# Optimization experiments

Measured on AMD Instinct MI355X. Metric: run time of the kernel, lower is better.

## Reference

```python
import jax, jax.numpy as jnp
import numpy as np

ANCHORS = [[(116, 90), (156, 198), (373, 326)],
           [(30, 61), (62, 45), (59, 119)],
           [(10, 13), (16, 30), (33, 23)]]
STRIDES = [32, 16, 8]
NC = 80            # num_classes
SCORE_THRESH = 0.01
NMS_THRESH = 0.45
TOPK = 200
PRE_NMS = 400


def _decode_level(feat, anchors, stride):
    # feat: [B, A*(NC+5), H, W]
    bs, C, H, W = feat.shape
    A = len(anchors)
    p = feat.reshape(bs, A, NC + 5, H, W).transpose(0, 1, 3, 4, 2)  # b a h w c
    gx = jnp.arange(W, dtype=feat.dtype)
    gy = jnp.arange(H, dtype=feat.dtype)
    aw = jnp.asarray([a[0] for a in anchors], feat.dtype)  # anchor w in pixels
    ah = jnp.asarray([a[1] for a in anchors], feat.dtype)
    # (sigmoid(x)+grid)*stride ; exp(w)*(anchor/stride)*stride = exp(w)*anchor
    bx = (jax.nn.sigmoid(p[..., 0]) + gx[None, None, None, :]) * stride
    by = (jax.nn.sigmoid(p[..., 1]) + gy[None, None, :, None]) * stride
    bw = jnp.exp(p[..., 2]) * aw[None, :, None, None]
    bh = jnp.exp(p[..., 3]) * ah[None, :, None, None]
    conf = jax.nn.sigmoid(p[..., 4])
    cls = jax.nn.sigmoid(p[..., 5:])
    out = jnp.concatenate([jnp.stack([bx, by, bw, bh, conf], -1), cls], -1)
    return out.reshape(bs, A * H * W, NC + 5)


def _iou_matrix(boxes):
    # boxes: [K,4] xyxy -> [K,K] IoU
    x1, y1, x2, y2 = boxes[:, 0], boxes[:, 1], boxes[:, 2], boxes[:, 3]
    area = jnp.maximum(x2 - x1, 0.0) * jnp.maximum(y2 - y1, 0.0)
    ix1 = jnp.maximum(x1[:, None], x1[None, :])
    iy1 = jnp.maximum(y1[:, None], y1[None, :])
    ix2 = jnp.minimum(x2[:, None], x2[None, :])
    iy2 = jnp.minimum(y2[:, None], y2[None, :])
    inter = jnp.maximum(ix2 - ix1, 0.0) * jnp.maximum(iy2 - iy1, 0.0)
    union = area[:, None] + area[None, :] - inter
    return inter / jnp.maximum(union, 1e-9)


def _nms_single(pred):
    # pred: [N, 5+NC] with xyxy boxes in cols 0:4, obj conf col 4, class probs 5:
    N = pred.shape[0]
    scores = pred[:, 4:5] * pred[:, 5:]                 # [N, NC]
    flat = scores.reshape(-1)                            # [N*NC]
    flat = jnp.where(flat >= SCORE_THRESH, flat, -1.0)   # low scores sink to bottom
    vals, idx = jax.lax.top_k(flat, PRE_NMS)             # [PRE_NMS]
    box_idx = idx // NC
    cls_idx = idx % NC
    boxes = pred[box_idx, :4]                            # [PRE_NMS, 4]
    valid = vals >= SCORE_THRESH

    iou = _iou_matrix(boxes)
    same_cls = cls_idx[:, None] == cls_idx[None, :]
    later = jnp.arange(PRE_NMS)[None, :] > jnp.arange(PRE_NMS)[:, None]
    sup_mat = (iou > NMS_THRESH) & same_cls & later      # [K,K] i suppresses j

    def body(i, keep):
        sup = sup_mat[i] & keep[i] & valid[i]
        return keep & (~sup)

    keep = jax.lax.fori_loop(0, PRE_NMS, body, jnp.ones(PRE_NMS, bool))
    keep = keep & valid

    final = jnp.where(keep, vals, -1.0)
    sel_scores, sel = jax.lax.top_k(final, TOPK)         # kept boxes, score-sorted
    pad = sel_scores < 0.0
    out_boxes = jnp.where(pad[:, None], 0.0, boxes[sel])
    out_scores = jnp.where(pad, 0.0, sel_scores)
    out_labels = jnp.where(pad, -1.0, cls_idx[sel].astype(pred.dtype))
    return jnp.concatenate([out_boxes, out_scores[:, None], out_labels[:, None]], -1)


def _forward(feat0, feat1, feat2):
    preds = [_decode_level(f, a, s) for f, a, s in
             zip((feat0, feat1, feat2), ANCHORS, STRIDES)]
    pred = jnp.concatenate(preds, axis=1)                # [B, Ntot, 5+NC]
    cx, cy, w, h = pred[..., 0], pred[..., 1], pred[..., 2], pred[..., 3]
    corners = jnp.stack([cx - w / 2, cy - h / 2, cx + w / 2, cy + h / 2], -1)
    pred = jnp.concatenate([corners, pred[..., 4:]], -1)
    return jax.vmap(_nms_single)(pred)                   # [B, TOPK, 6]


def setup_inputs() -> dict:
    key = jax.random.key(0)
    k0, k1, k2 = jax.random.split(key, 3)
    return {
        "feat0": jax.random.normal(k0, (8, 255, 19, 19), jnp.float32),
        "feat1": jax.random.normal(k1, (8, 255, 38, 38), jnp.float32),
        "feat2": jax.random.normal(k2, (8, 255, 76, 76), jnp.float32),
    }


def reference(feat0, feat1, feat2):
    return _forward(feat0, feat1, feat2)
```

## Files before the change

kernel.cpp:

```cpp
#include <hip/hip_runtime.h>
#include <stdint.h>

#define NB      22743
#define L0N     1083
#define L1N     5415
#define PRE     400
#define TOPK_N  200
#define CAP     2048
#define NBATCH  8
#define NBINS1  2048
#define NBINS2  4096
#define MIN_VALID_P9 (0xBC23D70Au >> 9)

typedef unsigned long long u64;
typedef unsigned int u32;

__device__ __forceinline__ float sigf(float x) { return 1.0f / (1.0f + expf(-x)); }

__device__ __forceinline__ u32 mono32(float f) {
    u32 u = __float_as_uint(f);
    return (u & 0x80000000u) ? ~u : (u | 0x80000000u);
}
__device__ __forceinline__ float unmono(u32 m) {
    u32 u = (m & 0x80000000u) ? (m & 0x7FFFFFFFu) : ~m;
    return __uint_as_float(u);
}

__device__ __forceinline__ const float* box_base(
    const float* f0, const float* f1, const float* f2,
    int b, int g, int* HW, int* cw, int* ch, float* stride, float* aw, float* ah)
{
    const float* f; int W, off, li;
    if (g < L0N)      { f = f0; W = 19; off = 0;   li = 0; *stride = 32.f; }
    else if (g < L1N) { f = f1; W = 38; off = L0N; li = 1; *stride = 16.f; }
    else              { f = f2; W = 76; off = L1N; li = 2; *stride = 8.f;  }
    const float AWt[3][3] = {{116.f,156.f,373.f},{30.f,62.f,59.f},{10.f,16.f,33.f}};
    const float AHt[3][3] = {{90.f,198.f,326.f},{61.f,45.f,119.f},{13.f,30.f,23.f}};
    int hw = W * W;
    int local = g - off;
    int a = local / hw; int r = local - a * hw;
    int h = r / W; int w = r - h * W;
    *HW = hw; *cw = w; *ch = h;
    *aw = AWt[li][a]; *ah = AHt[li][a];
    return f + (size_t)((b * 255 + a * 85) * hw + h * W + w);
}

template<int MODE>
__global__ void score_pass(const float* __restrict__ f0, const float* __restrict__ f1,
                           const float* __restrict__ f2,
                           u32* __restrict__ ghist, const int2* __restrict__ sel1,
                           const u32* __restrict__ t23, u32* __restrict__ cnt,
                           u64* __restrict__ cand)
{
    __shared__ u32 h[(MODE == 0) ? NBINS1 * 4 : ((MODE == 1) ? NBINS2 : 1)];
    const int b = blockIdx.y;
    const int tid = threadIdx.x;
    if (MODE == 0) { for (int i = tid; i < NBINS1 * 4; i += 256) h[i] = 0; __syncthreads(); }
    if (MODE == 1) { for (int i = tid; i < NBINS2; i += 256) h[i] = 0; __syncthreads(); }

    const int g = blockIdx.x * blockDim.x + tid;
    if (g < NB) {
        int HW, cw, ch; float stride, aw, ah;
        const float* p = box_base(f0, f1, f2, b, g, &HW, &cw, &ch, &stride, &aw, &ah);
        float conf = sigf(p[4 * HW]);
        u32 b1 = 0, T = 0;
        if (MODE == 1) b1 = (u32)sel1[b].x;
        if (MODE == 2) T = t23[b];
        bool do_box;
        if (MODE == 0)      do_box = (conf >= 0.01f);
        else if (MODE == 1) do_box = ((mono32(conf) >> 21) >= b1);
        else                do_box = ((mono32(conf) >> 9)  >= T);
        if (do_box) {
            for (int c = 0; c < 80; ++c) {
                float s = conf * sigf(p[(5 + c) * HW]);
                if (s < 0.01f) continue;
                u32 m = mono32(s);
                if (MODE == 0) {
                    atomicAdd(&h[(m >> 21) * 4 + (tid & 3)], 1u);
                } else if (MODE == 1) {
                    if ((m >> 21) == b1) atomicAdd(&h[(m >> 9) & 0xFFFu], 1u);
                } else {
                    if ((m >> 9) >= T) {
                        u32 pos = atomicAdd(&cnt[b], 1u);
                        if (pos < CAP) {
                            u32 e = (u32)(g * 80 + c);
                            cand[b * CAP + pos] = ((u64)m << 32) | (u64)(0xFFFFFFFFu - e);
                        }
                    }
                }
            }
        }
    }
    if (MODE == 0) {
        __syncthreads();
        u32* gh = ghist + b * NBINS1;
        for (int i = tid; i < NBINS1; i += 256) {
            u32 s = h[i*4] + h[i*4+1] + h[i*4+2] + h[i*4+3];
            if (s) atomicAdd(&gh[i], s);
        }
    }
    if (MODE == 1) {
        __syncthreads();
        u32* gh = ghist + b * NBINS2;
        for (int i = tid; i < NBINS2; i += 256)
            if (h[i]) atomicAdd(&gh[i], h[i]);
    }
}

template<int LEVEL>
__global__ __launch_bounds__(256) void scan_k(const u32* __restrict__ ghist,
                                              int2* __restrict__ sel1,
                                              u32* __restrict__ t23)
{
    constexpr int NB_ = (LEVEL == 1) ? NBINS1 : NBINS2;
    constexpr int CH  = NB_ / 256;
    const int b = blockIdx.x;
    const int tid = threadIdx.x;
    const u32* h = ghist + b * NB_;
    __shared__ u32 lh[NB_];
    __shared__ u32 part[256];
    __shared__ u32 suf[256];

    const u32 need = (LEVEL == 1) ? (u32)PRE : (u32)(PRE - sel1[b].y);

    for (int i = tid; i < NB_; i += 256) lh[i] = h[i];
    if (tid == 0) {
        if (LEVEL == 1) sel1[b] = make_int2(0, 0);
        else            t23[b]  = MIN_VALID_P9;
    }
    __syncthreads();

    u32 ps = 0;
    #pragma unroll
    for (int i = 0; i < CH; ++i) ps += lh[tid * CH + i];
    part[tid] = ps;
    __syncthreads();

    if (tid == 0) {
        u32 cum = 0;
        for (int t = 255; t >= 0; --t) { suf[t] = cum; cum += part[t]; }
    }
    __syncthreads();

    if (suf[tid] < need && suf[tid] + part[tid] >= need) {
        u32 cum = suf[tid];
        for (int bin = tid * CH + CH - 1; bin >= tid * CH; --bin) {
            u32 c = lh[bin];
            if (cum + c >= need) {
                if (LEVEL == 1) {
                    sel1[b] = make_int2(bin, (int)cum);
                } else {
                    u32 t = ((u32)sel1[b].x << 12) | (u32)bin;
                    t23[b] = (t > MIN_VALID_P9) ? t : MIN_VALID_P9;
                }
                break;
            }
            cum += c;
        }
    }
}

__global__ __launch_bounds__(512) void sortdec_k(
    const float* __restrict__ f0, const float* __restrict__ f1, const float* __restrict__ f2,
    const u32* __restrict__ cnt, const u64* __restrict__ cand,
    float4* __restrict__ DB, float* __restrict__ VALG, int* __restrict__ CLSG,
    u64* __restrict__ VBMG)
{
    __shared__ u64 keys[CAP];
    __shared__ u64 SKEY[PRE];
    const int b = blockIdx.x;
    const int tid = threadIdx.x;
    const int n = (int)min(cnt[b], (u32)CAP);

    for (int i = tid; i < n; i += 512) keys[i] = cand[b * CAP + i];
    for (int i = tid; i < PRE; i += 512) SKEY[i] = 0ull;
    __syncthreads();

    for (int e = tid; e < n; e += 512) {
        u64 my = keys[e];
        int r = 0, k = 0;
        for (; k + 4 <= n; k += 4)
            r += (int)(keys[k] > my) + (int)(keys[k+1] > my)
               + (int)(keys[k+2] > my) + (int)(keys[k+3] > my);
        for (; k < n; ++k) r += (int)(keys[k] > my);
        if (r < PRE) SKEY[r] = my;
    }
    __syncthreads();

    const int i = tid;
    bool valid = false;
    if (i < PRE) {
        u64 kk = SKEY[i];
        float v; int g, c;
        if (kk) {
            u32 m = (u32)(kk >> 32);
            u32 e = 0xFFFFFFFFu - (u32)(kk & 0xFFFFFFFFu);
            v = unmono(m); g = (int)(e / 80u); c = (int)(e - (u32)g * 80u);
            valid = true;
        } else { v = -1.0f; g = 0; c = 0; }
        int HW, cw, ch; float stride, aw, ah;
        const float* p = box_base(f0, f1, f2, b, g, &HW, &cw, &ch, &stride, &aw, &ah);
        float cx = (sigf(p[0])  + (float)cw) * stride;
        float cy = (sigf(p[HW]) + (float)ch) * stride;
        float bw = expf(p[2 * HW]) * aw;
        float bh = expf(p[3 * HW]) * ah;
        DB[b * PRE + i] = make_float4(cx - bw * 0.5f, cy - bh * 0.5f,
                                      cx + bw * 0.5f, cy + bh * 0.5f);
        VALG[b * PRE + i] = v;
        CLSG[b * PRE + i] = c;
    }
    u64 bal = __ballot(valid);
    if ((tid & 63) == 0 && (tid >> 6) < 7) VBMG[b * 8 + (tid >> 6)] = bal;
}

__global__ __launch_bounds__(256) void sup_k(const float4* __restrict__ DB,
                                             const int* __restrict__ CLSG,
                                             u64* __restrict__ SUPG)
{
    __shared__ float4 BX[PRE];
    __shared__ int LC[PRE];
    const int w = blockIdx.x, b = blockIdx.y;
    const int tid = threadIdx.x;
    for (int i = tid; i < PRE; i += 256) { BX[i] = DB[b * PRE + i]; LC[i] = CLSG[b * PRE + i]; }
    __syncthreads();

    const int jbase = w << 6;
    const int j1 = (jbase + 64 < PRE) ? (jbase + 64) : PRE;
    for (int i = tid; i < PRE; i += 256) {
        u64 mask = 0ull;
        if (w >= (i >> 6)) {
            float4 bi = BX[i]; int ci = LC[i];
            float ai = fmaxf(bi.z - bi.x, 0.f) * fmaxf(bi.w - bi.y, 0.f);
            for (int j = jbase; j < j1; ++j) {
                float4 bj = BX[j];
                bool ok = (LC[j] == ci) && (j > i);
                float ix1 = fmaxf(bi.x, bj.x), iy1 = fmaxf(bi.y, bj.y);
                float ix2 = fminf(bi.z, bj.z), iy2 = fminf(bi.w, bj.w);
                float inter = fmaxf(ix2 - ix1, 0.f) * fmaxf(iy2 - iy1, 0.f);
                float aj = fmaxf(bj.z - bj.x, 0.f) * fmaxf(bj.w - bj.y, 0.f);
                float iou = inter / fmaxf(ai + aj - inter, 1e-9f);
                if (ok && iou > 0.45f) mask |= 1ull << (j - jbase);
            }
        }
        SUPG[(b * PRE + i) * 7 + w] = mask;
    }
}

__global__ __launch_bounds__(256) void nms_out_k(
    const u64* __restrict__ SUPG, const u64* __restrict__ VBMG,
    const float4* __restrict__ DB, const float* __restrict__ VALG,
    const int* __restrict__ CLSG, float* __restrict__ out)
{
    __shared__ u64 SUP[PRE][7];
    __shared__ float4 BX[PRE];
    __shared__ float VALs[PRE];
    __shared__ int LC[PRE];
    __shared__ u64 VBM[8];
    __shared__ u64 KBM[8];

    const int b = blockIdx.x;
    const int tid = threadIdx.x;

    for (int t = tid; t < PRE * 7; t += 256) ((u64*)SUP)[t] = SUPG[b * PRE * 7 + t];
    for (int i = tid; i < PRE; i += 256) {
        BX[i] = DB[b * PRE + i]; VALs[i] = VALG[b * PRE + i]; LC[i] = CLSG[b * PRE + i];
    }
    if (tid < 8) { VBM[tid] = (tid < 7) ? VBMG[b * 8 + tid] : 0ull; KBM[tid] = 0ull; }
    __syncthreads();

    if (tid == 0) {
        u64 kp[7], A[7], B[7];
        #pragma unroll
        for (int w = 0; w < 7; ++w) kp[w] = VBM[w];
        #pragma unroll
        for (int w = 0; w < 7; ++w) A[w] = SUP[0][w];
        #pragma unroll
        for (int w = 0; w < 7; ++w) B[w] = SUP[1][w];
        #pragma unroll
        for (int w = 0; w < 7; ++w) {
            const int base = w << 6;
            const int lim = (w == 6) ? 16 : 64;
            for (int bi = 0; bi < lim; bi += 2) {
                int i = base + bi;
                if ((kp[w] >> bi) & 1) {
                    #pragma unroll
                    for (int w2 = 0; w2 < 7; ++w2) kp[w2] &= ~A[w2];
                }
                int ip2 = (i + 2 < PRE) ? (i + 2) : (PRE - 1);
                #pragma unroll
                for (int w2 = 0; w2 < 7; ++w2) A[w2] = SUP[ip2][w2];
                if ((kp[w] >> (bi + 1)) & 1) {
                    #pragma unroll
                    for (int w2 = 0; w2 < 7; ++w2) kp[w2] &= ~B[w2];
                }
                int ip3 = (i + 3 < PRE) ? (i + 3) : (PRE - 1);
                #pragma unroll
                for (int w2 = 0; w2 < 7; ++w2) B[w2] = SUP[ip3][w2];
            }
        }
        #pragma unroll
        for (int w = 0; w < 7; ++w) KBM[w] = kp[w];
    }
    __syncthreads();

    int totk = 0;
    #pragma unroll
    for (int w = 0; w < 7; ++w) totk += __popcll(KBM[w]);
    for (int j = tid; j < PRE; j += 256) {
        int w = j >> 6, bi = j & 63;
        int pre_kept = 0;
        for (int ww = 0; ww < w; ++ww) pre_kept += __popcll(KBM[ww]);
        u64 kw = KBM[w];
        pre_kept += __popcll(kw & ((1ull << bi) - 1ull));
        bool kept = (kw >> bi) & 1;
        int slot = kept ? pre_kept : (totk + j - pre_kept);
        if (slot < TOPK_N) {
            float* o = out + ((size_t)b * TOPK_N + slot) * 6;
            if (kept) {
                float4 bx = BX[j];
                o[0] = bx.x; o[1] = bx.y; o[2] = bx.z; o[3] = bx.w;
                o[4] = VALs[j]; o[5] = (float)LC[j];
            } else {
                o[0] = 0.f; o[1] = 0.f; o[2] = 0.f; o[3] = 0.f; o[4] = 0.f; o[5] = -1.f;
            }
        }
    }
}

extern "C" void kernel_launch(void* const* d_in, const int* in_sizes, int n_in,
                              void* d_out, int out_size, void* d_ws, size_t ws_size,
                              hipStream_t stream)
{
    const float* f0 = (const float*)d_in[0];
    const float* f1 = (const float*)d_in[1];
    const float* f2 = (const float*)d_in[2];
    float* out = (float*)d_out;
    char* ws = (char*)d_ws;

    u32*    ghist1 = (u32*)(ws);
    u32*    ghist2 = (u32*)(ws + 65536);
    u32*    cnt    = (u32*)(ws + 196608);
    int2*   sel1   = (int2*)(ws + 196640);
    u32*    t23    = (u32*)(ws + 196704);
    u64*    VBMG   = (u64*)(ws + 196736);
    u64*    cand   = (u64*)(ws + 197248);
    float4* DB     = (float4*)(ws + 328320);
    float*  VALG   = (float*)(ws + 379520);
    int*    CLSG   = (int*)(ws + 392320);
    u64*    SUPG   = (u64*)(ws + 405120);

    hipMemsetAsync(ws, 0, 196640, stream);

    dim3 grid((NB + 255) / 256, NBATCH);
    score_pass<0><<<grid, 256, 0, stream>>>(f0, f1, f2, ghist1, sel1, t23, cnt, cand);
    scan_k<1><<<NBATCH, 256, 0, stream>>>(ghist1, sel1, t23);
    score_pass<1><<<grid, 256, 0, stream>>>(f0, f1, f2, ghist2, sel1, t23, cnt, cand);
    scan_k<2><<<NBATCH, 256, 0, stream>>>(ghist2, sel1, t23);
    score_pass<2><<<grid, 256, 0, stream>>>(f0, f1, f2, ghist1, sel1, t23, cnt, cand);
    sortdec_k<<<NBATCH, 512, 0, stream>>>(f0, f1, f2, cnt, cand, DB, VALG, CLSG, VBMG);
    sup_k<<<dim3(7, NBATCH), 256, 0, stream>>>(DB, CLSG, SUPG);
    nms_out_k<<<NBATCH, 256, 0, stream>>>(SUPG, VBMG, DB, VALG, CLSG, out);
}
```

Measured before the change: 312.3 us.

## Prefilter boxes by objectness to bound threshold search, fuse final NMS kernels

Adds a per-batch objectness-confidence selection that keeps the top ~2560 boxes, scores only their 80 classes to find a safe lower bound on the 400th score, and uses that bound to gate the full histogram passes so most boxes skip the class loop. The sort/decode, suppression-mask and NMS output kernels are merged into one per-batch kernel that keeps everything in shared memory, removing global round-trips and launches. It adds two extra small kernels and relies on the prefilter bound being valid, since the product score never exceeds objectness. Suppression-mask work now runs on only 8 blocks instead of 56, which reduces parallelism there.

```diff
diff --git a/kernel.cpp b/kernel.cpp
--- a/kernel.cpp
+++ b/kernel.cpp
@@ -7,10 +7,13 @@
 #define PRE     400
 #define TOPK_N  200
 #define CAP     2048
+#define CAPC    2560
+#define NCONF   2560
 #define NBATCH  8
 #define NBINS1  2048
 #define NBINS2  4096
-#define MIN_VALID_P9 (0xBC23D70Au >> 9)
+#define MIN_VALID_P21 ((u32)(0xBC23D70Au >> 21))
+#define MIN_VALID_P9  ((u32)(0xBC23D70Au >> 9))
 
 typedef unsigned long long u64;
 typedef unsigned int u32;
@@ -45,61 +48,178 @@
     return f + (size_t)((b * 255 + a * 85) * hw + h * W + w);
 }
 
+__global__ __launch_bounds__(1024) void conf_select_k(
+    const float* __restrict__ f0, const float* __restrict__ f1,
+    const float* __restrict__ f2, int* __restrict__ BOXL, u32* __restrict__ cntc)
+{
+    __shared__ u32 h[NBINS1 * 2];
+    __shared__ u32 part[1024];
+    __shared__ u32 selbin;
+    __shared__ u32 lcnt;
+    const int b = blockIdx.x;
+    const int tid = threadIdx.x;
+    for (int i = tid; i < NBINS1 * 2; i += 1024) h[i] = 0;
+    if (tid == 0) { selbin = 0; lcnt = 0; }
+    __syncthreads();
+
+    for (int g = tid; g < NB; g += 1024) {
+        int HW, cw, ch; float stride, aw, ah;
+        const float* p = box_base(f0, f1, f2, b, g, &HW, &cw, &ch, &stride, &aw, &ah);
+        float conf = sigf(p[4 * HW]);
+        if (conf >= 0.01f)
+            atomicAdd(&h[(mono32(conf) >> 21) * 2 + (tid & 1)], 1u);
+    }
+    __syncthreads();
+
+    part[tid] = h[(tid*2)*2] + h[(tid*2)*2+1] + h[(tid*2+1)*2] + h[(tid*2+1)*2+1];
+    __syncthreads();
+    if (tid == 0) {
+        u32 cum = 0;
+        for (int t = 1023; t >= 0; --t) {
+            u32 c = part[t];
+            if (cum + c >= NCONF) {
+                u32 cb1 = h[(t*2+1)*2] + h[(t*2+1)*2+1];
+                selbin = (cum + cb1 >= NCONF) ? (u32)(t*2+1) : (u32)(t*2);
+                break;
+            }
+            cum += c;
+        }
+    }
+    __syncthreads();
+
+    const u32 Tc = selbin;
+    for (int g = tid; g < NB; g += 1024) {
+        int HW, cw, ch; float stride, aw, ah;
+        const float* p = box_base(f0, f1, f2, b, g, &HW, &cw, &ch, &stride, &aw, &ah);
+        float conf = sigf(p[4 * HW]);
+        if (conf >= 0.01f && (mono32(conf) >> 21) >= Tc) {
+            u32 pos = atomicAdd(&lcnt, 1u);
+            if (pos < CAPC) BOXL[b * CAPC + pos] = g;
+        }
+    }
+    __syncthreads();
+    if (tid == 0) cntc[b] = (lcnt < CAPC) ? lcnt : CAPC;
+}
+
+__global__ __launch_bounds__(256) void subset_score_k(
+    const float* __restrict__ f0, const float* __restrict__ f1,
+    const float* __restrict__ f2, const int* __restrict__ BOXL,
+    const u32* __restrict__ cntc, u32* __restrict__ ghist0)
+{
+    __shared__ u32 h[NBINS1];
+    const int b = blockIdx.y;
+    const int tid = threadIdx.x;
+    for (int i = tid; i < NBINS1; i += 256) h[i] = 0;
+    __syncthreads();
+
+    const int idx = blockIdx.x * 256 + tid;
+    const int lp = idx / 80, c = idx - lp * 80;
+    const int nlist = (int)min(cntc[b], (u32)CAPC);
+    if (lp < nlist) {
+        int g = BOXL[b * CAPC + lp];
+        int HW, cw, ch; float stride, aw, ah;
+        const float* p = box_base(f0, f1, f2, b, g, &HW, &cw, &ch, &stride, &aw, &ah);
+        float conf = sigf(p[4 * HW]);
+        float s = conf * sigf(p[(5 + c) * HW]);
+        if (s >= 0.01f) atomicAdd(&h[mono32(s) >> 21], 1u);
+    }
+    __syncthreads();
+    u32* gh = ghist0 + b * NBINS1;
+    for (int i = tid; i < NBINS1; i += 256)
+        if (h[i]) atomicAdd(&gh[i], h[i]);
+}
+
+__global__ __launch_bounds__(256) void subset_scan_k(const u32* __restrict__ ghist0,
+                                                     u32* __restrict__ P21)
+{
+    const int b = blockIdx.x;
+    const int tid = threadIdx.x;
+    const u32* h = ghist0 + b * NBINS1;
+    __shared__ u32 lh[NBINS1];
+    __shared__ u32 part[256];
+    __shared__ u32 suf[256];
+
+    for (int i = tid; i < NBINS1; i += 256) lh[i] = h[i];
+    if (tid == 0) P21[b] = MIN_VALID_P21;
+    __syncthreads();
+
+    u32 ps = 0;
+    #pragma unroll
+    for (int i = 0; i < 8; ++i) ps += lh[tid * 8 + i];
+    part[tid] = ps;
+    __syncthreads();
+    if (tid == 0) {
+        u32 cum = 0;
+        for (int t = 255; t >= 0; --t) { suf[t] = cum; cum += part[t]; }
+    }
+    __syncthreads();
+    if (suf[tid] < PRE && suf[tid] + part[tid] >= PRE) {
+        u32 cum = suf[tid];
+        for (int bin = tid * 8 + 7; bin >= tid * 8; --bin) {
+            u32 c = lh[bin];
+            if (cum + c >= PRE) {
+                P21[b] = ((u32)bin > MIN_VALID_P21) ? (u32)bin : MIN_VALID_P21;
+                break;
+            }
+            cum += c;
+        }
+    }
+}
+
 template<int MODE>
-__global__ void score_pass(const float* __restrict__ f0, const float* __restrict__ f1,
-                           const float* __restrict__ f2,
-                           u32* __restrict__ ghist, const int2* __restrict__ sel1,
-                           const u32* __restrict__ t23, u32* __restrict__ cnt,
-                           u64* __restrict__ cand)
-{
-    __shared__ u32 h[(MODE == 0) ? NBINS1 * 4 : ((MODE == 1) ? NBINS2 : 1)];
+__global__ __launch_bounds__(256) void gated_pass(
+    const float* __restrict__ f0, const float* __restrict__ f1,
+    const float* __restrict__ f2, const u32* __restrict__ P21,
+    const int2* __restrict__ sel1, const u32* __restrict__ t23,
+    u32* __restrict__ ghist, u32* __restrict__ cnt, u64* __restrict__ cand)
+{
+    __shared__ u32 h[(MODE == 1) ? NBINS1 : ((MODE == 2) ? NBINS2 : 1)];
     const int b = blockIdx.y;
     const int tid = threadIdx.x;
-    if (MODE == 0) { for (int i = tid; i < NBINS1 * 4; i += 256) h[i] = 0; __syncthreads(); }
-    if (MODE == 1) { for (int i = tid; i < NBINS2; i += 256) h[i] = 0; __syncthreads(); }
-
-    const int g = blockIdx.x * blockDim.x + tid;
+    if (MODE == 1) { for (int i = tid; i < NBINS1; i += 256) h[i] = 0; __syncthreads(); }
+    if (MODE == 2) { for (int i = tid; i < NBINS2; i += 256) h[i] = 0; __syncthreads(); }
+
+    const int g = blockIdx.x * 256 + tid;
     if (g < NB) {
         int HW, cw, ch; float stride, aw, ah;
         const float* p = box_base(f0, f1, f2, b, g, &HW, &cw, &ch, &stride, &aw, &ah);
         float conf = sigf(p[4 * HW]);
-        u32 b1 = 0, T = 0;
-        if (MODE == 1) b1 = (u32)sel1[b].x;
-        if (MODE == 2) T = t23[b];
-        bool do_box;
-        if (MODE == 0)      do_box = (conf >= 0.01f);
-        else if (MODE == 1) do_box = ((mono32(conf) >> 21) >= b1);
-        else                do_box = ((mono32(conf) >> 9)  >= T);
-        if (do_box) {
-            for (int c = 0; c < 80; ++c) {
-                float s = conf * sigf(p[(5 + c) * HW]);
-                if (s < 0.01f) continue;
-                u32 m = mono32(s);
-                if (MODE == 0) {
-                    atomicAdd(&h[(m >> 21) * 4 + (tid & 3)], 1u);
-                } else if (MODE == 1) {
-                    if ((m >> 21) == b1) atomicAdd(&h[(m >> 9) & 0xFFFu], 1u);
-                } else {
-                    if ((m >> 9) >= T) {
-                        u32 pos = atomicAdd(&cnt[b], 1u);
-                        if (pos < CAP) {
-                            u32 e = (u32)(g * 80 + c);
-                            cand[b * CAP + pos] = ((u64)m << 32) | (u64)(0xFFFFFFFFu - e);
+        if (conf >= 0.01f) {
+            u32 mc = mono32(conf);
+            u32 gate1 = 0, T = 0;
+            bool do_box;
+            if (MODE == 1)      { gate1 = P21[b];          do_box = ((mc >> 21) >= gate1); }
+            else if (MODE == 2) { gate1 = (u32)sel1[b].x;  do_box = ((mc >> 21) >= gate1); }
+            else                { T = t23[b];              do_box = ((mc >> 9)  >= T); }
+            if (do_box) {
+                for (int c = 0; c < 80; ++c) {
+                    float s = conf * sigf(p[(5 + c) * HW]);
+                    if (s < 0.01f) continue;
+                    u32 m = mono32(s);
+                    if (MODE == 1) {
+                        atomicAdd(&h[m >> 21], 1u);
+                    } else if (MODE == 2) {
+                        if ((m >> 21) == gate1) atomicAdd(&h[(m >> 9) & 0xFFFu], 1u);
+                    } else {
+                        if ((m >> 9) >= T) {
+                            u32 pos = atomicAdd(&cnt[b], 1u);
+                            if (pos < CAP) {
+                                u32 e = (u32)(g * 80 + c);
+                                cand[b * CAP + pos] = ((u64)m << 32) | (u64)(0xFFFFFFFFu - e);
+                            }
                         }
                     }
                 }
             }
         }
     }
-    if (MODE == 0) {
+    if (MODE == 1) {
         __syncthreads();
         u32* gh = ghist + b * NBINS1;
-        for (int i = tid; i < NBINS1; i += 256) {
-            u32 s = h[i*4] + h[i*4+1] + h[i*4+2] + h[i*4+3];
-            if (s) atomicAdd(&gh[i], s);
-        }
-    }
-    if (MODE == 1) {
+        for (int i = tid; i < NBINS1; i += 256)
+            if (h[i]) atomicAdd(&gh[i], h[i]);
+    }
+    if (MODE == 2) {
         __syncthreads();
         u32* gh = ghist + b * NBINS2;
         for (int i = tid; i < NBINS2; i += 256)
@@ -160,20 +280,27 @@
     }
 }
 
-__global__ __launch_bounds__(512) void sortdec_k(
-    const float* __restrict__ f0, const float* __restrict__ f1, const float* __restrict__ f2,
-    const u32* __restrict__ cnt, const u64* __restrict__ cand,
-    float4* __restrict__ DB, float* __restrict__ VALG, int* __restrict__ CLSG,
-    u64* __restrict__ VBMG)
+__global__ __launch_bounds__(512) void fused_final_k(
+    const float* __restrict__ f0, const float* __restrict__ f1,
+    const float* __restrict__ f2, const u32* __restrict__ cnt,
+    const u64* __restrict__ cand, float* __restrict__ out)
 {
     __shared__ u64 keys[CAP];
     __shared__ u64 SKEY[PRE];
+    __shared__ float4 BX[PRE];
+    __shared__ float VALs[PRE];
+    __shared__ int LC[PRE];
+    __shared__ u64 SUP[PRE][7];
+    __shared__ u64 VBM[8];
+    __shared__ u64 KBM[8];
+
     const int b = blockIdx.x;
     const int tid = threadIdx.x;
     const int n = (int)min(cnt[b], (u32)CAP);
 
     for (int i = tid; i < n; i += 512) keys[i] = cand[b * CAP + i];
     for (int i = tid; i < PRE; i += 512) SKEY[i] = 0ull;
+    if (tid < 8) { VBM[tid] = 0ull; KBM[tid] = 0ull; }
     __syncthreads();
 
     for (int e = tid; e < n; e += 512) {
@@ -187,10 +314,9 @@
     }
     __syncthreads();
 
-    const int i = tid;
     bool valid = false;
-    if (i < PRE) {
-        u64 kk = SKEY[i];
+    if (tid < PRE) {
+        u64 kk = SKEY[tid];
         float v; int g, c;
         if (kk) {
             u32 m = (u32)(kk >> 32);
@@ -198,74 +324,44 @@
             v = unmono(m); g = (int)(e / 80u); c = (int)(e - (u32)g * 80u);
             valid = true;
         } else { v = -1.0f; g = 0; c = 0; }
+        VALs[tid] = v; LC[tid] = c;
         int HW, cw, ch; float stride, aw, ah;
         const float* p = box_base(f0, f1, f2, b, g, &HW, &cw, &ch, &stride, &aw, &ah);
         float cx = (sigf(p[0])  + (float)cw) * stride;
         float cy = (sigf(p[HW]) + (float)ch) * stride;
         float bw = expf(p[2 * HW]) * aw;
         float bh = expf(p[3 * HW]) * ah;
-        DB[b * PRE + i] = make_float4(cx - bw * 0.5f, cy - bh * 0.5f,
-                                      cx + bw * 0.5f, cy + bh * 0.5f);
-        VALG[b * PRE + i] = v;
-        CLSG[b * PRE + i] = c;
+        BX[tid] = make_float4(cx - bw * 0.5f, cy - bh * 0.5f,
+                              cx + bw * 0.5f, cy + bh * 0.5f);
     }
     u64 bal = __ballot(valid);
-    if ((tid & 63) == 0 && (tid >> 6) < 7) VBMG[b * 8 + (tid >> 6)] = bal;
-}
-
-__global__ __launch_bounds__(256) void sup_k(const float4* __restrict__ DB,
-                                             const int* __restrict__ CLSG,
-                                             u64* __restrict__ SUPG)
-{
-    __shared__ float4 BX[PRE];
-    __shared__ int LC[PRE];
-    const int w = blockIdx.x, b = blockIdx.y;
-    const int tid = threadIdx.x;
-    for (int i = tid; i < PRE; i += 256) { BX[i] = DB[b * PRE + i]; LC[i] = CLSG[b * PRE + i]; }
-    __syncthreads();
-
-    const int jbase = w << 6;
-    const int j1 = (jbase + 64 < PRE) ? (jbase + 64) : PRE;
-    for (int i = tid; i < PRE; i += 256) {
-        u64 mask = 0ull;
-        if (w >= (i >> 6)) {
-            float4 bi = BX[i]; int ci = LC[i];
-            float ai = fmaxf(bi.z - bi.x, 0.f) * fmaxf(bi.w - bi.y, 0.f);
-            for (int j = jbase; j < j1; ++j) {
-                float4 bj = BX[j];
-                bool ok = (LC[j] == ci) && (j > i);
-                float ix1 = fmaxf(bi.x, bj.x), iy1 = fmaxf(bi.y, bj.y);
-                float ix2 = fminf(bi.z, bj.z), iy2 = fminf(bi.w, bj.w);
-                float inter = fmaxf(ix2 - ix1, 0.f) * fmaxf(iy2 - iy1, 0.f);
-                float aj = fmaxf(bj.z - bj.x, 0.f) * fmaxf(bj.w - bj.y, 0.f);
-                float iou = inter / fmaxf(ai + aj - inter, 1e-9f);
-                if (ok && iou > 0.45f) mask |= 1ull << (j - jbase);
-            }
-        }
-        SUPG[(b * PRE + i) * 7 + w] = mask;
-    }
-}
-
-__global__ __launch_bounds__(256) void nms_out_k(
-    const u64* __restrict__ SUPG, const u64* __restrict__ VBMG,
-    const float4* __restrict__ DB, const float* __restrict__ VALG,
-    const int* __restrict__ CLSG, float* __restrict__ out)
-{
-    __shared__ u64 SUP[PRE][7];
-    __shared__ float4 BX[PRE];
-    __shared__ float VALs[PRE];
-    __shared__ int LC[PRE];
-    __shared__ u64 VBM[8];
-    __shared__ u64 KBM[8];
-
-    const int b = blockIdx.x;
-    const int tid = threadIdx.x;
-
-    for (int t = tid; t < PRE * 7; t += 256) ((u64*)SUP)[t] = SUPG[b * PRE * 7 + t];
-    for (int i = tid; i < PRE; i += 256) {
-        BX[i] = DB[b * PRE + i]; VALs[i] = VALG[b * PRE + i]; LC[i] = CLSG[b * PRE + i];
-    }
-    if (tid < 8) { VBM[tid] = (tid < 7) ? VBMG[b * 8 + tid] : 0ull; KBM[tid] = 0ull; }
+    if ((tid & 63) == 0 && (tid >> 6) < 7) VBM[tid >> 6] = bal;
+    __syncthreads();
+
+    if (tid < PRE) {
+        const int i = tid;
+        float4 bi = BX[i]; int ci = LC[i];
+        float ai = fmaxf(bi.z - bi.x, 0.f) * fmaxf(bi.w - bi.y, 0.f);
+        #pragma unroll
+        for (int w = 0; w < 7; ++w) {
+            u64 mask = 0ull;
+            if (w >= (i >> 6)) {
+                int jbase = w << 6;
+                int j1 = (jbase + 64 < PRE) ? (jbase + 64) : PRE;
+                for (int j = jbase; j < j1; ++j) {
+                    float4 bj = BX[j];
+                    bool ok = (LC[j] == ci) && (j > i);
+                    float ix1 = fmaxf(bi.x, bj.x), iy1 = fmaxf(bi.y, bj.y);
+                    float ix2 = fminf(bi.z, bj.z), iy2 = fminf(bi.w, bj.w);
+                    float inter = fmaxf(ix2 - ix1, 0.f) * fmaxf(iy2 - iy1, 0.f);
+                    float aj = fmaxf(bj.z - bj.x, 0.f) * fmaxf(bj.w - bj.y, 0.f);
+                    float iou = inter / fmaxf(ai + aj - inter, 1e-9f);
+                    if (ok && iou > 0.45f) mask |= 1ull << (j - jbase);
+                }
+            }
+            SUP[i][w] = mask;
+        }
+    }
     __syncthreads();
 
     if (tid == 0) {
@@ -306,7 +402,7 @@
     int totk = 0;
     #pragma unroll
     for (int w = 0; w < 7; ++w) totk += __popcll(KBM[w]);
-    for (int j = tid; j < PRE; j += 256) {
+    for (int j = tid; j < PRE; j += 512) {
         int w = j >> 6, bi = j & 63;
         int pre_kept = 0;
         for (int ww = 0; ww < w; ++ww) pre_kept += __popcll(KBM[ww]);
@@ -337,27 +433,28 @@
     float* out = (float*)d_out;
     char* ws = (char*)d_ws;
 
-    u32*    ghist1 = (u32*)(ws);
-    u32*    ghist2 = (u32*)(ws + 65536);
-    u32*    cnt    = (u32*)(ws + 196608);
-    int2*   sel1   = (int2*)(ws + 196640);
-    u32*    t23    = (u32*)(ws + 196704);
-    u64*    VBMG   = (u64*)(ws + 196736);
-    u64*    cand   = (u64*)(ws + 197248);
-    float4* DB     = (float4*)(ws + 328320);
-    float*  VALG   = (float*)(ws + 379520);
-    int*    CLSG   = (int*)(ws + 392320);
-    u64*    SUPG   = (u64*)(ws + 405120);
-
-    hipMemsetAsync(ws, 0, 196640, stream);
-
-    dim3 grid((NB + 255) / 256, NBATCH);
-    score_pass<0><<<grid, 256, 0, stream>>>(f0, f1, f2, ghist1, sel1, t23, cnt, cand);
+    u32*  ghist0 = (u32*)(ws);
+    u32*  ghist1 = (u32*)(ws + 65536);
+    u32*  ghist2 = (u32*)(ws + 131072);
+    u32*  cntc   = (u32*)(ws + 262144);
+    u32*  cnt    = (u32*)(ws + 262176);
+    u32*  P21    = (u32*)(ws + 262208);
+    u32*  t23    = (u32*)(ws + 262240);
+    int2* sel1   = (int2*)(ws + 262272);
+    int*  BOXL   = (int*)(ws + 262336);
+    u64*  cand   = (u64*)(ws + 344256);
+
+    hipMemsetAsync(ws, 0, 262208, stream);
+
+    dim3 gridNB((NB + 255) / 256, NBATCH);
+    conf_select_k<<<NBATCH, 1024, 0, stream>>>(f0, f1, f2, BOXL, cntc);
+    subset_score_k<<<dim3(CAPC * 80 / 256, NBATCH), 256, 0, stream>>>(
+        f0, f1, f2, BOXL, cntc, ghist0);
+    subset_scan_k<<<NBATCH, 256, 0, stream>>>(ghist0, P21);
+    gated_pass<1><<<gridNB, 256, 0, stream>>>(f0, f1, f2, P21, sel1, t23, ghist1, cnt, cand);
     scan_k<1><<<NBATCH, 256, 0, stream>>>(ghist1, sel1, t23);
-    score_pass<1><<<grid, 256, 0, stream>>>(f0, f1, f2, ghist2, sel1, t23, cnt, cand);
+    gated_pass<2><<<gridNB, 256, 0, stream>>>(f0, f1, f2, P21, sel1, t23, ghist2, cnt, cand);
     scan_k<2><<<NBATCH, 256, 0, stream>>>(ghist2, sel1, t23);
-    score_pass<2><<<grid, 256, 0, stream>>>(f0, f1, f2, ghist1, sel1, t23, cnt, cand);
-    sortdec_k<<<NBATCH, 512, 0, stream>>>(f0, f1, f2, cnt, cand, DB, VALG, CLSG, VBMG);
-    sup_k<<<dim3(7, NBATCH), 256, 0, stream>>>(DB, CLSG, SUPG);
-    nms_out_k<<<NBATCH, 256, 0, stream>>>(SUPG, VBMG, DB, VALG, CLSG, out);
-}
+    gated_pass<3><<<gridNB, 256, 0, stream>>>(f0, f1, f2, P21, sel1, t23, ghist1, cnt, cand);
+    fused_final_k<<<NBATCH, 512, 0, stream>>>(f0, f1, f2, cnt, cand, out);
+}
```

Measured after the change: 403.6 us. 1.29x slower.
